# Performance work log

Measured on AMD Instinct MI355X. Metric: run time of the kernel, lower is better.

Reference implementation:

```python
import jax, jax.numpy as jnp
import numpy as np

C = 512

def _conv1x1(x, w, b):
    # x: [B, C, T], w: [O, C], b: [O] -> [B, O, T]
    return jnp.einsum('oc,bct->bot', w, x) + b[None, :, None]

def setup_inputs() -> dict:
    key = jax.random.key(0)
    ks = jax.random.split(key, 9)
    B, T = 8, 2048
    s = 1.0 / np.sqrt(C)
    inp = {'x': jax.random.normal(ks[0], (B, C, T), dtype=jnp.float32)}
    names = ['theta', 'phi', 'g', 'w']
    for i, n in enumerate(names):
        inp[f'w_{n}'] = jax.random.uniform(ks[1 + 2 * i], (C, C), jnp.float32, -s, s)
        inp[f'b_{n}'] = jax.random.uniform(ks[2 + 2 * i], (C,), jnp.float32, -s, s)
    return inp

def reference(x, w_theta, b_theta, w_phi, b_phi, w_g, b_g, w_w, b_w):
    relu = jax.nn.relu
    feat_theta = relu(_conv1x1(x, w_theta, b_theta))          # [B, C, T]
    feat_phi = relu(_conv1x1(x, w_phi, b_phi))                # [B, C, T]
    # scores: Q^T K over channel dim -> [B, T, T]
    scores = jnp.einsum('bci,bcj->bij', feat_theta, feat_phi)
    attn = jax.nn.softmax(scores, axis=2)                     # [B, T, T]
    feat_g = relu(_conv1x1(x, w_g, b_g))                      # [B, C, T]
    # attention-weighted V: [B, T, T] x [B, T, C] -> [B, T, C] -> [B, C, T]
    feature = jnp.einsum('bij,bcj->bci', attn, feat_g)
    w_feature = relu(_conv1x1(feature, w_w, b_w))
    return w_feature + x
```

## Files before the change

kernel.cpp:

```cpp
#include <hip/hip_runtime.h>
#include <math.h>

#define C_DIM 512
#define T_DIM 2048
#define B_DIM 8

typedef _Float16 f16;
typedef __attribute__((ext_vector_type(8))) _Float16 half8;
typedef __attribute__((ext_vector_type(4))) _Float16 half4;
typedef __attribute__((ext_vector_type(4))) float floatx4;

__global__ __launch_bounds__(256) void convert_w_kernel(
    const float* __restrict__ w0, const float* __restrict__ w1,
    const float* __restrict__ w2, const float* __restrict__ w3,
    f16* __restrict__ o0, f16* __restrict__ o1,
    f16* __restrict__ o2, f16* __restrict__ o3)
{
    const float* src; f16* dst;
    switch (blockIdx.z) {
        case 0:  src = w0; dst = o0; break;
        case 1:  src = w1; dst = o1; break;
        case 2:  src = w2; dst = o2; break;
        default: src = w3; dst = o3; break;
    }
    const int idx = (blockIdx.x * 256 + threadIdx.x) * 4;
    const float4 v = *(const float4*)(src + idx);
    half4 h; h[0] = (f16)v.x; h[1] = (f16)v.y; h[2] = (f16)v.z; h[3] = (f16)v.w;
    *(half4*)(dst + idx) = h;
}

__global__ __launch_bounds__(256) void concat_bias_kernel(
    const float* __restrict__ b0, const float* __restrict__ b1,
    float* __restrict__ o)
{
    const int i = blockIdx.x * 256 + threadIdx.x;
    o[i] = (i < 512) ? b0[i] : b1[i - 512];
}

__global__ __launch_bounds__(256) void transpose_x_kernel(
    const float* __restrict__ x, f16* __restrict__ xt)
{
    __shared__ float xs[32][33];
    const int b  = blockIdx.z;
    const int t0 = blockIdx.x * 32, c0 = blockIdx.y * 32;
    const float* xb = x + (size_t)b * C_DIM * T_DIM;
    const int r = threadIdx.x >> 3, q = threadIdx.x & 7;

    const float4 v = *(const float4*)(xb + (size_t)(c0 + r) * T_DIM + t0 + q * 4);
    xs[r][q * 4 + 0] = v.x; xs[r][q * 4 + 1] = v.y;
    xs[r][q * 4 + 2] = v.z; xs[r][q * 4 + 3] = v.w;
    __syncthreads();

    f16* xtb = xt + (size_t)b * C_DIM * T_DIM;
    half4 h;
    h[0] = (f16)xs[q * 4 + 0][r]; h[1] = (f16)xs[q * 4 + 1][r];
    h[2] = (f16)xs[q * 4 + 2][r]; h[3] = (f16)xs[q * 4 + 3][r];
    *(half4*)(xtb + (size_t)(t0 + r) * C_DIM + c0 + q * 4) = h;
}

template<int MODE>
__global__ __launch_bounds__(256) void gemm_tn(
    const f16* __restrict__ A, size_t sA, int lda,
    const f16* __restrict__ B, size_t sB, int ldb,
    void* __restrict__ Cp, size_t sC, int ldc,
    const float* __restrict__ bias,
    const float* __restrict__ resid, size_t sR,
    int K)
{
    __shared__ __align__(16) f16 As[2][128 * 32];
    __shared__ __align__(16) f16 Bs[2][128 * 32];

    const int gx = gridDim.x;
    const int flat = blockIdx.y * gx + blockIdx.x;
    const int jsc = gx >> 2;
    const int sh = (jsc <= 1) ? 0 : (31 - __builtin_clz(jsc));
    const int s = flat >> 4, rem = flat & 15;
    const int i0 = ((s >> sh) * 4 + (rem >> 2)) * 128;
    const int j0 = (((jsc <= 1) ? 0 : (s & (jsc - 1))) * 4 + (rem & 3)) * 128;

    const int bz = blockIdx.z;
    A += (size_t)bz * sA;
    B += (size_t)bz * sB;

    const int tid  = threadIdx.x;
    const int lane = tid & 63;
    const int wave = tid >> 6;
    const int wy = wave >> 1, wx = wave & 1;
    const int quad = lane >> 4, l16 = lane & 15;

    const int row1 = tid >> 2, ch = tid & 3;
    const int row2 = row1 + 64;
    const int w1 = row1 * 32 + ((ch ^ (row1 & 3)) << 3);
    const int w2 = row2 * 32 + ((ch ^ (row2 & 3)) << 3);

    const f16* gA1 = A + (size_t)(i0 + row1) * lda + ch * 8;
    const f16* gA2 = A + (size_t)(i0 + row2) * lda + ch * 8;
    const f16* gB1 = B + (size_t)(j0 + row1) * ldb + ch * 8;
    const f16* gB2 = B + (size_t)(j0 + row2) * ldb + ch * 8;

    const int xa = (quad ^ (l16 & 3)) << 3;

    const int nt = K >> 5;

    float4 a1_0 = *(const float4*)(gA1);      float4 a2_0 = *(const float4*)(gA2);
    float4 b1_0 = *(const float4*)(gB1);      float4 b2_0 = *(const float4*)(gB2);
    float4 a1_1 = *(const float4*)(gA1 + 32); float4 a2_1 = *(const float4*)(gA2 + 32);
    float4 b1_1 = *(const float4*)(gB1 + 32); float4 b2_1 = *(const float4*)(gB2 + 32);

    floatx4 acc[4][4] = {};

    for (int t = 0; t < nt; t += 2) {
        *(float4*)&As[0][w1] = a1_0;
        *(float4*)&As[0][w2] = a2_0;
        *(float4*)&Bs[0][w1] = b1_0;
        *(float4*)&Bs[0][w2] = b2_0;
        if (t + 2 < nt) {
            const int off = (t + 2) * 32;
            a1_0 = *(const float4*)(gA1 + off); a2_0 = *(const float4*)(gA2 + off);
            b1_0 = *(const float4*)(gB1 + off); b2_0 = *(const float4*)(gB2 + off);
        }
        __syncthreads();
        {
            half8 af[4], bf[4];
            #pragma unroll
            for (int mi = 0; mi < 4; ++mi)
                af[mi] = *(const half8*)&As[0][(wy * 64 + mi * 16 + l16) * 32 + xa];
            #pragma unroll
            for (int ni = 0; ni < 4; ++ni)
                bf[ni] = *(const half8*)&Bs[0][(wx * 64 + ni * 16 + l16) * 32 + xa];
            #pragma unroll
            for (int mi = 0; mi < 4; ++mi)
                #pragma unroll
                for (int ni = 0; ni < 4; ++ni)
                    acc[mi][ni] = __builtin_amdgcn_mfma_f32_16x16x32_f16(
                        af[mi], bf[ni], acc[mi][ni], 0, 0, 0);
        }
        *(float4*)&As[1][w1] = a1_1;
        *(float4*)&As[1][w2] = a2_1;
        *(float4*)&Bs[1][w1] = b1_1;
        *(float4*)&Bs[1][w2] = b2_1;
        if (t + 3 < nt) {
            const int off = (t + 3) * 32;
            a1_1 = *(const float4*)(gA1 + off); a2_1 = *(const float4*)(gA2 + off);
            b1_1 = *(const float4*)(gB1 + off); b2_1 = *(const float4*)(gB2 + off);
        }
        __syncthreads();
        {
            half8 af[4], bf[4];
            #pragma unroll
            for (int mi = 0; mi < 4; ++mi)
                af[mi] = *(const half8*)&As[1][(wy * 64 + mi * 16 + l16) * 32 + xa];
            #pragma unroll
            for (int ni = 0; ni < 4; ++ni)
                bf[ni] = *(const half8*)&Bs[1][(wx * 64 + ni * 16 + l16) * 32 + xa];
            #pragma unroll
            for (int mi = 0; mi < 4; ++mi)
                #pragma unroll
                for (int ni = 0; ni < 4; ++ni)
                    acc[mi][ni] = __builtin_amdgcn_mfma_f32_16x16x32_f16(
                        af[mi], bf[ni], acc[mi][ni], 0, 0, 0);
        }
    }

    #pragma unroll
    for (int mi = 0; mi < 4; ++mi) {
        #pragma unroll
        for (int ni = 0; ni < 4; ++ni) {
            const int col = j0 + wx * 64 + ni * 16 + l16;
            #pragma unroll
            for (int r = 0; r < 4; ++r) {
                const int row = i0 + wy * 64 + mi * 16 + quad * 4 + r;
                float v = acc[mi][ni][r];
                if (MODE == 1) { v += bias[col]; v = v > 0.f ? v : 0.f; }
                if (MODE == 2) { v += bias[row]; v = v > 0.f ? v : 0.f; }
                if (MODE == 3) {
                    v += bias[row];
                    v = v > 0.f ? v : 0.f;
                    v += resid[(size_t)bz * sR + (size_t)row * ldc + col];
                    ((float*)Cp)[(size_t)bz * sC + (size_t)row * ldc + col] = v;
                } else {
                    ((f16*)Cp)[(size_t)bz * sC + (size_t)row * ldc + col] = (f16)v;
                }
            }
        }
    }
}

__global__ __launch_bounds__(256) void softmax_f16_kernel(f16* __restrict__ S)
{
    f16* p = S + (size_t)blockIdx.x * T_DIM;
    const int tid = threadIdx.x;

    half8 hv = *((const half8*)p + tid);
    float v[8];
    float lmax = -1e30f;
    #pragma unroll
    for (int c = 0; c < 8; ++c) { v[c] = (float)hv[c]; lmax = fmaxf(lmax, v[c]); }
    #pragma unroll
    for (int off = 32; off; off >>= 1)
        lmax = fmaxf(lmax, __shfl_down(lmax, off));
    __shared__ float redm[4];
    if ((tid & 63) == 0) redm[tid >> 6] = lmax;
    __syncthreads();
    const float m = fmaxf(fmaxf(redm[0], redm[1]), fmaxf(redm[2], redm[3]));

    float lsum = 0.f;
    #pragma unroll
    for (int c = 0; c < 8; ++c) { v[c] = __expf(v[c] - m); lsum += v[c]; }
    #pragma unroll
    for (int off = 32; off; off >>= 1)
        lsum += __shfl_down(lsum, off);
    __shared__ float reds[4];
    if ((tid & 63) == 0) reds[tid >> 6] = lsum;
    __syncthreads();
    const float inv = 1.f / (reds[0] + reds[1] + reds[2] + reds[3]);

    #pragma unroll
    for (int c = 0; c < 8; ++c) hv[c] = (f16)(v[c] * inv);
    *((half8*)p + tid) = hv;
}

extern "C" void kernel_launch(void* const* d_in, const int* in_sizes, int n_in,
                              void* d_out, int out_size, void* d_ws, size_t ws_size,
                              hipStream_t stream)
{
    const float* x       = (const float*)d_in[0];
    const float* w_theta = (const float*)d_in[1];
    const float* b_theta = (const float*)d_in[2];
    const float* w_phi   = (const float*)d_in[3];
    const float* b_phi   = (const float*)d_in[4];
    const float* w_g     = (const float*)d_in[5];
    const float* b_g     = (const float*)d_in[6];
    const float* w_w     = (const float*)d_in[7];
    const float* b_w     = (const float*)d_in[8];
    float* out = (float*)d_out;

    const size_t FE = (size_t)B_DIM * C_DIM * T_DIM;
    const size_t TC = (size_t)T_DIM * C_DIM;
    const size_t TT = (size_t)T_DIM * T_DIM;

    f16* xt      = (f16*)d_ws;
    f16* wtp     = xt + FE;
    f16* wg_h    = wtp + 524288;
    f16* ww_h    = wg_h + 262144;
    float* btp   = (float*)(ww_h + 262144);
    f16* tp      = (f16*)(btp + 1024);
    f16* g       = tp + (size_t)B_DIM * T_DIM * 1024;
    f16* scores  = g + FE;
    f16* feature = tp;

    const dim3 blk(256);

    convert_w_kernel<<<dim3(256, 1, 4), blk, 0, stream>>>(
        w_theta, w_phi, w_g, w_w, wtp, wtp + 262144, wg_h, ww_h);
    concat_bias_kernel<<<dim3(4), blk, 0, stream>>>(b_theta, b_phi, btp);
    transpose_x_kernel<<<dim3(T_DIM / 32, C_DIM / 32, B_DIM), blk, 0, stream>>>(x, xt);

    gemm_tn<1><<<dim3(1024 / 128, T_DIM / 128, B_DIM), blk, 0, stream>>>(
        xt, TC, C_DIM, wtp, 0, C_DIM, tp, (size_t)T_DIM * 1024, 1024,
        btp, nullptr, 0, C_DIM);
    gemm_tn<2><<<dim3(T_DIM / 128, C_DIM / 128, B_DIM), blk, 0, stream>>>(
        wg_h, 0, C_DIM, xt, TC, C_DIM, g, TC, T_DIM, b_g, nullptr, 0, C_DIM);
    gemm_tn<0><<<dim3(T_DIM / 128, T_DIM / 128, B_DIM), blk, 0, stream>>>(
        tp, (size_t)T_DIM * 1024, 1024, tp + 512, (size_t)T_DIM * 1024, 1024,
        scores, TT, T_DIM, nullptr, nullptr, 0, C_DIM);
    softmax_f16_kernel<<<dim3(B_DIM * T_DIM), blk, 0, stream>>>(scores);
    gemm_tn<0><<<dim3(C_DIM / 128, T_DIM / 128, B_DIM), blk, 0, stream>>>(
        scores, TT, T_DIM, g, TC, T_DIM, feature, TC, C_DIM, nullptr, nullptr, 0, T_DIM);
    gemm_tn<3><<<dim3(T_DIM / 128, C_DIM / 128, B_DIM), blk, 0, stream>>>(
        ww_h, 0, C_DIM, feature, TC, C_DIM, out, TC, T_DIM, b_w, x, TC, C_DIM);
}
```

Baseline: 274.1 us.

## Fuse softmax into score GEMM partial stats and PV GEMM A-load

Removes the standalone softmax pass over the scores matrix. The score GEMM epilogue now writes per-tile row max and exp-sum partials, a small merge kernel reduces them to per-row max and inverse denominator, and the PV GEMM applies exp and normalisation while staging A tiles into shared memory. It also replaces the block-index swizzle with an XCD-aware region mapping. This saves one full read and write of the fp16 scores, in exchange for extra exp work in the PV GEMM's load path and an epilogue reduction in the score GEMM.

```diff
diff --git a/kernel.cpp b/kernel.cpp
--- a/kernel.cpp
+++ b/kernel.cpp
@@ -58,25 +58,38 @@
     *(half4*)(xtb + (size_t)(t0 + r) * C_DIM + c0 + q * 4) = h;
 }
 
-template<int MODE>
+__device__ __forceinline__ float4 exp_stage(float4 raw, float M, float iD) {
+    half8 h = *(half8*)&raw;
+    half8 o;
+    #pragma unroll
+    for (int c = 0; c < 8; ++c)
+        o[c] = (f16)(__expf((float)h[c] - M) * iD);
+    return *(float4*)&o;
+}
+
+template<int MODE, int PART, int EXPA>
 __global__ __launch_bounds__(256) void gemm_tn(
     const f16* __restrict__ A, size_t sA, int lda,
     const f16* __restrict__ B, size_t sB, int ldb,
     void* __restrict__ Cp, size_t sC, int ldc,
     const float* __restrict__ bias,
     const float* __restrict__ resid, size_t sR,
-    int K)
+    int K, int RI, int RJ,
+    float2* __restrict__ part, const float2* __restrict__ rowstat)
 {
     __shared__ __align__(16) f16 As[2][128 * 32];
     __shared__ __align__(16) f16 Bs[2][128 * 32];
 
     const int gx = gridDim.x;
     const int flat = blockIdx.y * gx + blockIdx.x;
-    const int jsc = gx >> 2;
-    const int sh = (jsc <= 1) ? 0 : (31 - __builtin_clz(jsc));
-    const int s = flat >> 4, rem = flat & 15;
-    const int i0 = ((s >> sh) * 4 + (rem >> 2)) * 128;
-    const int j0 = (((jsc <= 1) ? 0 : (s & (jsc - 1))) * 4 + (rem & 3)) * 128;
+    const int per_xcd = (gx * gridDim.y) >> 3;
+    const int region = flat & 7;
+    const int idx = flat >> 3;
+    const int NRJ = gx / RJ;
+    const int rI = region / NRJ, rJ = region % NRJ;
+    const int ii = idx / RJ, jj = idx % RJ;
+    const int i0 = (rI * RI + ii) * 128;
+    const int j0 = (rJ * RJ + jj) * 128;
 
     const int bz = blockIdx.z;
     A += (size_t)bz * sA;
@@ -98,6 +111,13 @@
     const f16* gB1 = B + (size_t)(j0 + row1) * ldb + ch * 8;
     const f16* gB2 = B + (size_t)(j0 + row2) * ldb + ch * 8;
 
+    float M1 = 0.f, iD1 = 0.f, M2 = 0.f, iD2 = 0.f;
+    if (EXPA) {
+        const float2 s1 = rowstat[bz * T_DIM + i0 + row1];
+        const float2 s2 = rowstat[bz * T_DIM + i0 + row2];
+        M1 = s1.x; iD1 = s1.y; M2 = s2.x; iD2 = s2.y;
+    }
+
     const int xa = (quad ^ (l16 & 3)) << 3;
 
     const int nt = K >> 5;
@@ -110,8 +130,8 @@
     floatx4 acc[4][4] = {};
 
     for (int t = 0; t < nt; t += 2) {
-        *(float4*)&As[0][w1] = a1_0;
-        *(float4*)&As[0][w2] = a2_0;
+        *(float4*)&As[0][w1] = EXPA ? exp_stage(a1_0, M1, iD1) : a1_0;
+        *(float4*)&As[0][w2] = EXPA ? exp_stage(a2_0, M2, iD2) : a2_0;
         *(float4*)&Bs[0][w1] = b1_0;
         *(float4*)&Bs[0][w2] = b2_0;
         if (t + 2 < nt) {
@@ -135,8 +155,8 @@
                     acc[mi][ni] = __builtin_amdgcn_mfma_f32_16x16x32_f16(
                         af[mi], bf[ni], acc[mi][ni], 0, 0, 0);
         }
-        *(float4*)&As[1][w1] = a1_1;
-        *(float4*)&As[1][w2] = a2_1;
+        *(float4*)&As[1][w1] = EXPA ? exp_stage(a1_1, M1, iD1) : a1_1;
+        *(float4*)&As[1][w2] = EXPA ? exp_stage(a2_1, M2, iD2) : a2_1;
         *(float4*)&Bs[1][w1] = b1_1;
         *(float4*)&Bs[1][w2] = b2_1;
         if (t + 3 < nt) {
@@ -184,40 +204,82 @@
             }
         }
     }
-}
-
-__global__ __launch_bounds__(256) void softmax_f16_kernel(f16* __restrict__ S)
-{
-    f16* p = S + (size_t)blockIdx.x * T_DIM;
-    const int tid = threadIdx.x;
-
-    half8 hv = *((const half8*)p + tid);
-    float v[8];
-    float lmax = -1e30f;
-    #pragma unroll
-    for (int c = 0; c < 8; ++c) { v[c] = (float)hv[c]; lmax = fmaxf(lmax, v[c]); }
-    #pragma unroll
-    for (int off = 32; off; off >>= 1)
-        lmax = fmaxf(lmax, __shfl_down(lmax, off));
-    __shared__ float redm[4];
-    if ((tid & 63) == 0) redm[tid >> 6] = lmax;
-    __syncthreads();
-    const float m = fmaxf(fmaxf(redm[0], redm[1]), fmaxf(redm[2], redm[3]));
-
-    float lsum = 0.f;
-    #pragma unroll
-    for (int c = 0; c < 8; ++c) { v[c] = __expf(v[c] - m); lsum += v[c]; }
-    #pragma unroll
-    for (int off = 32; off; off >>= 1)
-        lsum += __shfl_down(lsum, off);
-    __shared__ float reds[4];
-    if ((tid & 63) == 0) reds[tid >> 6] = lsum;
-    __syncthreads();
-    const float inv = 1.f / (reds[0] + reds[1] + reds[2] + reds[3]);
-
-    #pragma unroll
-    for (int c = 0; c < 8; ++c) hv[c] = (f16)(v[c] * inv);
-    *((half8*)p + tid) = hv;
+
+    if (PART) {
+        float* red = (float*)As;
+        __syncthreads();
+
+        float rmax[4][4];
+        #pragma unroll
+        for (int mi = 0; mi < 4; ++mi)
+            #pragma unroll
+            for (int r = 0; r < 4; ++r) {
+                float v = fmaxf(fmaxf(acc[mi][0][r], acc[mi][1][r]),
+                                fmaxf(acc[mi][2][r], acc[mi][3][r]));
+                #pragma unroll
+                for (int off = 1; off < 16; off <<= 1)
+                    v = fmaxf(v, __shfl_xor(v, off));
+                if (l16 == 0)
+                    red[(((wy * 2 + wx) * 4 + mi) * 4 + quad) * 4 + r] = v;
+                rmax[mi][r] = v;
+            }
+        __syncthreads();
+        #pragma unroll
+        for (int mi = 0; mi < 4; ++mi)
+            #pragma unroll
+            for (int r = 0; r < 4; ++r)
+                rmax[mi][r] = fmaxf(
+                    red[(((wy * 2 + 0) * 4 + mi) * 4 + quad) * 4 + r],
+                    red[(((wy * 2 + 1) * 4 + mi) * 4 + quad) * 4 + r]);
+        __syncthreads();
+        float* red2 = red + 256;
+        #pragma unroll
+        for (int mi = 0; mi < 4; ++mi)
+            #pragma unroll
+            for (int r = 0; r < 4; ++r) {
+                float s = __expf(acc[mi][0][r] - rmax[mi][r])
+                        + __expf(acc[mi][1][r] - rmax[mi][r])
+                        + __expf(acc[mi][2][r] - rmax[mi][r])
+                        + __expf(acc[mi][3][r] - rmax[mi][r]);
+                #pragma unroll
+                for (int off = 1; off < 16; off <<= 1)
+                    s += __shfl_xor(s, off);
+                if (l16 == 0)
+                    red2[(((wy * 2 + wx) * 4 + mi) * 4 + quad) * 4 + r] = s;
+            }
+        __syncthreads();
+        if (wx == 0 && l16 == 0) {
+            const int jt = j0 >> 7;
+            #pragma unroll
+            for (int mi = 0; mi < 4; ++mi)
+                #pragma unroll
+                for (int r = 0; r < 4; ++r) {
+                    const int row = i0 + wy * 64 + mi * 16 + quad * 4 + r;
+                    const float s =
+                        red2[(((wy * 2 + 0) * 4 + mi) * 4 + quad) * 4 + r] +
+                        red2[(((wy * 2 + 1) * 4 + mi) * 4 + quad) * 4 + r];
+                    part[((size_t)bz * gx + jt) * T_DIM + row] =
+                        make_float2(rmax[mi][r], s);
+                }
+        }
+    }
+}
+
+__global__ __launch_bounds__(256) void merge_rows_kernel(
+    const float2* __restrict__ part, float2* __restrict__ rowstat, int NJ)
+{
+    const int rid = blockIdx.x * 256 + threadIdx.x;
+    const int b = rid >> 11, i = rid & 2047;
+    const float2* p = part + (size_t)b * NJ * T_DIM + i;
+    float M = -1e30f;
+    for (int j = 0; j < NJ; ++j)
+        M = fmaxf(M, p[(size_t)j * T_DIM].x);
+    float D = 0.f;
+    for (int j = 0; j < NJ; ++j) {
+        const float2 v = p[(size_t)j * T_DIM];
+        D += v.y * __expf(v.x - M);
+    }
+    rowstat[rid] = make_float2(M, 1.f / D);
 }
 
 extern "C" void kernel_launch(void* const* d_in, const int* in_sizes, int n_in,
@@ -247,6 +309,8 @@
     f16* tp      = (f16*)(btp + 1024);
     f16* g       = tp + (size_t)B_DIM * T_DIM * 1024;
     f16* scores  = g + FE;
+    float2* part = (float2*)(scores + (size_t)B_DIM * TT);
+    float2* rowstat = part + (size_t)B_DIM * 16 * T_DIM;
     f16* feature = tp;
 
     const dim3 blk(256);
@@ -256,17 +320,21 @@
     concat_bias_kernel<<<dim3(4), blk, 0, stream>>>(b_theta, b_phi, btp);
     transpose_x_kernel<<<dim3(T_DIM / 32, C_DIM / 32, B_DIM), blk, 0, stream>>>(x, xt);
 
-    gemm_tn<1><<<dim3(1024 / 128, T_DIM / 128, B_DIM), blk, 0, stream>>>(
+    gemm_tn<1,0,0><<<dim3(8, 16, B_DIM), blk, 0, stream>>>(
         xt, TC, C_DIM, wtp, 0, C_DIM, tp, (size_t)T_DIM * 1024, 1024,
-        btp, nullptr, 0, C_DIM);
-    gemm_tn<2><<<dim3(T_DIM / 128, C_DIM / 128, B_DIM), blk, 0, stream>>>(
-        wg_h, 0, C_DIM, xt, TC, C_DIM, g, TC, T_DIM, b_g, nullptr, 0, C_DIM);
-    gemm_tn<0><<<dim3(T_DIM / 128, T_DIM / 128, B_DIM), blk, 0, stream>>>(
+        btp, nullptr, 0, C_DIM, 4, 4, nullptr, nullptr);
+    gemm_tn<2,0,0><<<dim3(16, 4, B_DIM), blk, 0, stream>>>(
+        wg_h, 0, C_DIM, xt, TC, C_DIM, g, TC, T_DIM,
+        b_g, nullptr, 0, C_DIM, 2, 4, nullptr, nullptr);
+    gemm_tn<0,1,0><<<dim3(16, 16, B_DIM), blk, 0, stream>>>(
         tp, (size_t)T_DIM * 1024, 1024, tp + 512, (size_t)T_DIM * 1024, 1024,
-        scores, TT, T_DIM, nullptr, nullptr, 0, C_DIM);
-    softmax_f16_kernel<<<dim3(B_DIM * T_DIM), blk, 0, stream>>>(scores);
-    gemm_tn<0><<<dim3(C_DIM / 128, T_DIM / 128, B_DIM), blk, 0, stream>>>(
-        scores, TT, T_DIM, g, TC, T_DIM, feature, TC, C_DIM, nullptr, nullptr, 0, T_DIM);
-    gemm_tn<3><<<dim3(T_DIM / 128, C_DIM / 128, B_DIM), blk, 0, stream>>>(
-        ww_h, 0, C_DIM, feature, TC, C_DIM, out, TC, T_DIM, b_w, x, TC, C_DIM);
-}
+        scores, TT, T_DIM, nullptr, nullptr, 0, C_DIM, 4, 8, part, nullptr);
+    merge_rows_kernel<<<dim3(B_DIM * T_DIM / 256), blk, 0, stream>>>(
+        part, rowstat, 16);
+    gemm_tn<0,0,1><<<dim3(4, 16, B_DIM), blk, 0, stream>>>(
+        scores, TT, T_DIM, g, TC, T_DIM, feature, TC, C_DIM,
+        nullptr, nullptr, 0, T_DIM, 2, 4, nullptr, rowstat);
+    gemm_tn<3,0,0><<<dim3(16, 4, B_DIM), blk, 0, stream>>>(
+        ww_h, 0, C_DIM, feature, TC, C_DIM, out, TC, T_DIM,
+        b_w, x, TC, C_DIM, 2, 4, nullptr, nullptr);
+}
```

Result: slower. 283.3 us (+3.3%).

## Templatize GEMM tile height, add region-based block swizzle, fuse prep kernels

Applied to the files above, without the earlier changes.

Makes the GEMM M-tile height a template parameter: 256 rows for the projection and score GEMMs, 128 for the rest. Block scheduling now groups tiles into eight regions with configurable RI/RJ extents for L2 locality, and launch bounds request two blocks per CU. The weight conversion, bias concat and x transpose kernels are merged into one launch to cut launch overhead. Larger tiles raise reuse per block but use more registers, with MI=8 needing 128 accumulator floats, so the two-blocks-per-CU target may cause spills or lower occupancy.

```diff
diff --git a/kernel.cpp b/kernel.cpp
--- a/kernel.cpp
+++ b/kernel.cpp
@@ -10,41 +10,43 @@
 typedef __attribute__((ext_vector_type(4))) _Float16 half4;
 typedef __attribute__((ext_vector_type(4))) float floatx4;
 
-__global__ __launch_bounds__(256) void convert_w_kernel(
+__global__ __launch_bounds__(256) void prep_kernel(
+    const float* __restrict__ x, f16* __restrict__ xt,
     const float* __restrict__ w0, const float* __restrict__ w1,
     const float* __restrict__ w2, const float* __restrict__ w3,
     f16* __restrict__ o0, f16* __restrict__ o1,
-    f16* __restrict__ o2, f16* __restrict__ o3)
-{
-    const float* src; f16* dst;
-    switch (blockIdx.z) {
-        case 0:  src = w0; dst = o0; break;
-        case 1:  src = w1; dst = o1; break;
-        case 2:  src = w2; dst = o2; break;
-        default: src = w3; dst = o3; break;
-    }
-    const int idx = (blockIdx.x * 256 + threadIdx.x) * 4;
-    const float4 v = *(const float4*)(src + idx);
-    half4 h; h[0] = (f16)v.x; h[1] = (f16)v.y; h[2] = (f16)v.z; h[3] = (f16)v.w;
-    *(half4*)(dst + idx) = h;
-}
-
-__global__ __launch_bounds__(256) void concat_bias_kernel(
+    f16* __restrict__ o2, f16* __restrict__ o3,
     const float* __restrict__ b0, const float* __restrict__ b1,
-    float* __restrict__ o)
-{
-    const int i = blockIdx.x * 256 + threadIdx.x;
-    o[i] = (i < 512) ? b0[i] : b1[i - 512];
-}
-
-__global__ __launch_bounds__(256) void transpose_x_kernel(
-    const float* __restrict__ x, f16* __restrict__ xt)
-{
+    float* __restrict__ btp)
+{
+    const int tid = threadIdx.x;
+    if (blockIdx.z == 8) {
+        const int idx = blockIdx.y * 64 + blockIdx.x;
+        const int wsel = idx >> 8, blk = idx & 255;
+        const float* src; f16* dst;
+        switch (wsel) {
+            case 0:  src = w0; dst = o0; break;
+            case 1:  src = w1; dst = o1; break;
+            case 2:  src = w2; dst = o2; break;
+            default: src = w3; dst = o3; break;
+        }
+        const int e = blk * 1024 + tid * 4;
+        const float4 v = *(const float4*)(src + e);
+        half4 h; h[0] = (f16)v.x; h[1] = (f16)v.y; h[2] = (f16)v.z; h[3] = (f16)v.w;
+        *(half4*)(dst + e) = h;
+        if (idx == 0) {
+            const int i = tid * 4;
+            const float4 bv = (i < 512) ? *(const float4*)(b0 + i)
+                                        : *(const float4*)(b1 + i - 512);
+            *(float4*)(btp + i) = bv;
+        }
+        return;
+    }
     __shared__ float xs[32][33];
     const int b  = blockIdx.z;
     const int t0 = blockIdx.x * 32, c0 = blockIdx.y * 32;
     const float* xb = x + (size_t)b * C_DIM * T_DIM;
-    const int r = threadIdx.x >> 3, q = threadIdx.x & 7;
+    const int r = tid >> 3, q = tid & 7;
 
     const float4 v = *(const float4*)(xb + (size_t)(c0 + r) * T_DIM + t0 + q * 4);
     xs[r][q * 4 + 0] = v.x; xs[r][q * 4 + 1] = v.y;
@@ -58,25 +60,29 @@
     *(half4*)(xtb + (size_t)(t0 + r) * C_DIM + c0 + q * 4) = h;
 }
 
-template<int MODE>
-__global__ __launch_bounds__(256) void gemm_tn(
+template<int MI, int MODE>
+__global__ __launch_bounds__(256, 2) void gemm_tn(
     const f16* __restrict__ A, size_t sA, int lda,
     const f16* __restrict__ B, size_t sB, int ldb,
     void* __restrict__ Cp, size_t sC, int ldc,
     const float* __restrict__ bias,
     const float* __restrict__ resid, size_t sR,
-    int K)
-{
-    __shared__ __align__(16) f16 As[2][128 * 32];
+    int K, int RI, int RJ)
+{
+    constexpr int BM = MI * 32;
+    constexpr int NA = MI / 2;
+    __shared__ __align__(16) f16 As[2][BM * 32];
     __shared__ __align__(16) f16 Bs[2][128 * 32];
 
     const int gx = gridDim.x;
     const int flat = blockIdx.y * gx + blockIdx.x;
-    const int jsc = gx >> 2;
-    const int sh = (jsc <= 1) ? 0 : (31 - __builtin_clz(jsc));
-    const int s = flat >> 4, rem = flat & 15;
-    const int i0 = ((s >> sh) * 4 + (rem >> 2)) * 128;
-    const int j0 = (((jsc <= 1) ? 0 : (s & (jsc - 1))) * 4 + (rem & 3)) * 128;
+    const int region = flat & 7;
+    const int idx = flat >> 3;
+    const int NRJ = gx / RJ;
+    const int rI = region / NRJ, rJ = region % NRJ;
+    const int ii = idx / RJ, jj = idx % RJ;
+    const int i0 = (rI * RI + ii) * BM;
+    const int j0 = (rJ * RJ + jj) * 128;
 
     const int bz = blockIdx.z;
     A += (size_t)bz * sA;
@@ -88,73 +94,84 @@
     const int wy = wave >> 1, wx = wave & 1;
     const int quad = lane >> 4, l16 = lane & 15;
 
-    const int row1 = tid >> 2, ch = tid & 3;
-    const int row2 = row1 + 64;
-    const int w1 = row1 * 32 + ((ch ^ (row1 & 3)) << 3);
-    const int w2 = row2 * 32 + ((ch ^ (row2 & 3)) << 3);
-
-    const f16* gA1 = A + (size_t)(i0 + row1) * lda + ch * 8;
-    const f16* gA2 = A + (size_t)(i0 + row2) * lda + ch * 8;
-    const f16* gB1 = B + (size_t)(j0 + row1) * ldb + ch * 8;
-    const f16* gB2 = B + (size_t)(j0 + row2) * ldb + ch * 8;
+    const int rowA = tid >> 2, ch = tid & 3;
+    const int slot = (ch ^ (rowA & 3)) << 3;
+    int wA[NA]; const f16* gA[NA];
+    #pragma unroll
+    for (int u = 0; u < NA; ++u) {
+        const int r = rowA + u * 64;
+        wA[u] = r * 32 + slot;
+        gA[u] = A + (size_t)(i0 + r) * lda + ch * 8;
+    }
+    const int wB1 = rowA * 32 + slot, wB2 = (rowA + 64) * 32 + slot;
+    const f16* gB1 = B + (size_t)(j0 + rowA) * ldb + ch * 8;
+    const f16* gB2 = B + (size_t)(j0 + rowA + 64) * ldb + ch * 8;
 
     const int xa = (quad ^ (l16 & 3)) << 3;
 
     const int nt = K >> 5;
 
-    float4 a1_0 = *(const float4*)(gA1);      float4 a2_0 = *(const float4*)(gA2);
-    float4 b1_0 = *(const float4*)(gB1);      float4 b2_0 = *(const float4*)(gB2);
-    float4 a1_1 = *(const float4*)(gA1 + 32); float4 a2_1 = *(const float4*)(gA2 + 32);
-    float4 b1_1 = *(const float4*)(gB1 + 32); float4 b2_1 = *(const float4*)(gB2 + 32);
-
-    floatx4 acc[4][4] = {};
+    float4 a0[NA], a1[NA], b0a, b0b, b1a, b1b;
+    #pragma unroll
+    for (int u = 0; u < NA; ++u) {
+        a0[u] = *(const float4*)(gA[u]);
+        a1[u] = *(const float4*)(gA[u] + 32);
+    }
+    b0a = *(const float4*)(gB1);      b0b = *(const float4*)(gB2);
+    b1a = *(const float4*)(gB1 + 32); b1b = *(const float4*)(gB2 + 32);
+
+    floatx4 acc[MI][4] = {};
 
     for (int t = 0; t < nt; t += 2) {
-        *(float4*)&As[0][w1] = a1_0;
-        *(float4*)&As[0][w2] = a2_0;
-        *(float4*)&Bs[0][w1] = b1_0;
-        *(float4*)&Bs[0][w2] = b2_0;
+        #pragma unroll
+        for (int u = 0; u < NA; ++u) *(float4*)&As[0][wA[u]] = a0[u];
+        *(float4*)&Bs[0][wB1] = b0a;
+        *(float4*)&Bs[0][wB2] = b0b;
         if (t + 2 < nt) {
             const int off = (t + 2) * 32;
-            a1_0 = *(const float4*)(gA1 + off); a2_0 = *(const float4*)(gA2 + off);
-            b1_0 = *(const float4*)(gB1 + off); b2_0 = *(const float4*)(gB2 + off);
+            #pragma unroll
+            for (int u = 0; u < NA; ++u) a0[u] = *(const float4*)(gA[u] + off);
+            b0a = *(const float4*)(gB1 + off);
+            b0b = *(const float4*)(gB2 + off);
         }
         __syncthreads();
         {
-            half8 af[4], bf[4];
-            #pragma unroll
-            for (int mi = 0; mi < 4; ++mi)
-                af[mi] = *(const half8*)&As[0][(wy * 64 + mi * 16 + l16) * 32 + xa];
+            half8 af[MI], bf[4];
+            #pragma unroll
+            for (int mi = 0; mi < MI; ++mi)
+                af[mi] = *(const half8*)&As[0][(wy * (MI * 16) + mi * 16 + l16) * 32 + xa];
             #pragma unroll
             for (int ni = 0; ni < 4; ++ni)
                 bf[ni] = *(const half8*)&Bs[0][(wx * 64 + ni * 16 + l16) * 32 + xa];
             #pragma unroll
-            for (int mi = 0; mi < 4; ++mi)
+            for (int mi = 0; mi < MI; ++mi)
                 #pragma unroll
                 for (int ni = 0; ni < 4; ++ni)
                     acc[mi][ni] = __builtin_amdgcn_mfma_f32_16x16x32_f16(
                         af[mi], bf[ni], acc[mi][ni], 0, 0, 0);
         }
-        *(float4*)&As[1][w1] = a1_1;
-        *(float4*)&As[1][w2] = a2_1;
-        *(float4*)&Bs[1][w1] = b1_1;
-        *(float4*)&Bs[1][w2] = b2_1;
+        #pragma unroll
+        for (int u = 0; u < NA; ++u) *(float4*)&As[1][wA[u]] = a1[u];
+        *(float4*)&Bs[1][wB1] = b1a;
+        *(float4*)&Bs[1][wB2] = b1b;
         if (t + 3 < nt) {
             const int off = (t + 3) * 32;
-            a1_1 = *(const float4*)(gA1 + off); a2_1 = *(const float4*)(gA2 + off);
-            b1_1 = *(const float4*)(gB1 + off); b2_1 = *(const float4*)(gB2 + off);
+            #pragma unroll
+            for (int u = 0; u < NA; ++u) a1[u] = *(const float4*)(gA[u] + off);
+            b1a = *(const float4*)(gB1 + off);
+            b1b = *(const float4*)(gB2 + off);
         }
         __syncthreads();
         {
-            half8 af[4], bf[4];
-            #pragma unroll
-            for (int mi = 0; mi < 4; ++mi)
-                af[mi] = *(const half8*)&As[1][(wy * 64 + mi * 16 + l16) * 32 + xa];
+            half8 af[MI], bf[4];
+            #pragma unroll
+            for (int mi = 0; mi < MI; ++mi)
+                af[mi] = *(const half8*)&As[1][(wy * (MI * 16) + mi * 16 + l16) * 32 + xa];
             #pragma unroll
             for (int ni = 0; ni < 4; ++ni)
                 bf[ni] = *(const half8*)&Bs[1][(wx * 64 + ni * 16 + l16) * 32 + xa];
             #pragma unroll
-            for (int mi = 0; mi < 4; ++mi)
+            for (int mi = 0; mi < MI; ++mi)
                 #pragma unroll
                 for (int ni = 0; ni < 4; ++ni)
                     acc[mi][ni] = __builtin_amdgcn_mfma_f32_16x16x32_f16(
@@ -163,13 +180,13 @@
     }
 
     #pragma unroll
-    for (int mi = 0; mi < 4; ++mi) {
+    for (int mi = 0; mi < MI; ++mi) {
         #pragma unroll
         for (int ni = 0; ni < 4; ++ni) {
             const int col = j0 + wx * 64 + ni * 16 + l16;
             #pragma unroll
             for (int r = 0; r < 4; ++r) {
-                const int row = i0 + wy * 64 + mi * 16 + quad * 4 + r;
+                const int row = i0 + wy * (MI * 16) + mi * 16 + quad * 4 + r;
                 float v = acc[mi][ni][r];
                 if (MODE == 1) { v += bias[col]; v = v > 0.f ? v : 0.f; }
                 if (MODE == 2) { v += bias[row]; v = v > 0.f ? v : 0.f; }
@@ -251,22 +268,24 @@
 
     const dim3 blk(256);
 
-    convert_w_kernel<<<dim3(256, 1, 4), blk, 0, stream>>>(
-        w_theta, w_phi, w_g, w_w, wtp, wtp + 262144, wg_h, ww_h);
-    concat_bias_kernel<<<dim3(4), blk, 0, stream>>>(b_theta, b_phi, btp);
-    transpose_x_kernel<<<dim3(T_DIM / 32, C_DIM / 32, B_DIM), blk, 0, stream>>>(x, xt);
-
-    gemm_tn<1><<<dim3(1024 / 128, T_DIM / 128, B_DIM), blk, 0, stream>>>(
+    prep_kernel<<<dim3(64, 16, 9), blk, 0, stream>>>(
+        x, xt, w_theta, w_phi, w_g, w_w,
+        wtp, wtp + 262144, wg_h, ww_h, b_theta, b_phi, btp);
+
+    gemm_tn<8, 1><<<dim3(8, 8, B_DIM), blk, 0, stream>>>(
         xt, TC, C_DIM, wtp, 0, C_DIM, tp, (size_t)T_DIM * 1024, 1024,
-        btp, nullptr, 0, C_DIM);
-    gemm_tn<2><<<dim3(T_DIM / 128, C_DIM / 128, B_DIM), blk, 0, stream>>>(
-        wg_h, 0, C_DIM, xt, TC, C_DIM, g, TC, T_DIM, b_g, nullptr, 0, C_DIM);
-    gemm_tn<0><<<dim3(T_DIM / 128, T_DIM / 128, B_DIM), blk, 0, stream>>>(
+        btp, nullptr, 0, C_DIM, 2, 4);
+    gemm_tn<4, 2><<<dim3(16, 4, B_DIM), blk, 0, stream>>>(
+        wg_h, 0, C_DIM, xt, TC, C_DIM, g, TC, T_DIM,
+        b_g, nullptr, 0, C_DIM, 1, 8);
+    gemm_tn<8, 0><<<dim3(16, 8, B_DIM), blk, 0, stream>>>(
         tp, (size_t)T_DIM * 1024, 1024, tp + 512, (size_t)T_DIM * 1024, 1024,
-        scores, TT, T_DIM, nullptr, nullptr, 0, C_DIM);
+        scores, TT, T_DIM, nullptr, nullptr, 0, C_DIM, 2, 8);
     softmax_f16_kernel<<<dim3(B_DIM * T_DIM), blk, 0, stream>>>(scores);
-    gemm_tn<0><<<dim3(C_DIM / 128, T_DIM / 128, B_DIM), blk, 0, stream>>>(
-        scores, TT, T_DIM, g, TC, T_DIM, feature, TC, C_DIM, nullptr, nullptr, 0, T_DIM);
-    gemm_tn<3><<<dim3(T_DIM / 128, C_DIM / 128, B_DIM), blk, 0, stream>>>(
-        ww_h, 0, C_DIM, feature, TC, C_DIM, out, TC, T_DIM, b_w, x, TC, C_DIM);
-}
+    gemm_tn<4, 0><<<dim3(4, 16, B_DIM), blk, 0, stream>>>(
+        scores, TT, T_DIM, g, TC, T_DIM, feature, TC, C_DIM,
+        nullptr, nullptr, 0, T_DIM, 4, 2);
+    gemm_tn<4, 3><<<dim3(16, 4, B_DIM), blk, 0, stream>>>(
+        ww_h, 0, C_DIM, feature, TC, C_DIM, out, TC, T_DIM,
+        b_w, x, TC, C_DIM, 1, 8);
+}
```

Result: slower. 432.0 us (+57.6%).
